# Performance work log

Hardware: AMD Instinct MI355X
Metric: run time of the kernel (lower is better)

The kernel has to match this reference:

```python
import jax, jax.numpy as jnp
import numpy as np

B, S, D, H = 2, 4096, 512, 8
DH = D // H  # head dim = 64


def setup_inputs() -> dict:
    key = jax.random.key(0)
    ks = jax.random.split(key, 5)
    s = 1.0 / np.sqrt(D)
    return {
        "x": jax.random.normal(ks[0], (B, S, D), jnp.float32),
        "Wq": jax.random.normal(ks[1], (D, D), jnp.float32) * s,
        "bq": jnp.zeros((D,), jnp.float32),
        "Wk": jax.random.normal(ks[2], (D, D), jnp.float32) * s,
        "bk": jnp.zeros((D,), jnp.float32),
        "Wv": jax.random.normal(ks[3], (D, D), jnp.float32) * s,
        "bv": jnp.zeros((D,), jnp.float32),
        "Wo": jax.random.normal(ks[4], (D, D), jnp.float32) * s,
        "bo": jnp.zeros((D,), jnp.float32),
    }


def _split_heads(t):  # [B,S,D] -> [B,H,S,DH]
    return t.reshape(B, S, H, DH).transpose(0, 2, 1, 3)


def reference(x, Wq, bq, Wk, bk, Wv, bv, Wo, bo):
    relu = jax.nn.relu
    # linear projections with activation (keras MultiHeadAttention applies
    # the activation to all Q/K/V/output mappings)
    q = _split_heads(relu(x @ Wq + bq))
    k = _split_heads(relu(x @ Wk + bk))
    v = _split_heads(relu(x @ Wv + bv))
    # scaled dot-product attention; scale uses per-head feature dim (DH)
    e = jnp.einsum("bhqd,bhkd->bhqk", q, k) / jnp.sqrt(jnp.float32(DH))
    attn = jax.nn.softmax(e, axis=-1)  # stable max-subtract softmax
    o = jnp.einsum("bhqk,bhkd->bhqd", attn, v)
    o = o.transpose(0, 2, 1, 3).reshape(B, S, D)  # merge heads
    return relu(o @ Wo + bo)
```

## Files before the change

### kernel.cpp

```cpp
#include <hip/hip_runtime.h>
#include <stdint.h>

#define B_ 2
#define S_ 4096
#define D_ 512
#define H_ 8
#define DH_ 64
#define M_ (B_*S_)
#define LOG2E 1.4426950408889634f

typedef unsigned short u16;
typedef __bf16 bf16x8 __attribute__((ext_vector_type(8)));
typedef __bf16 bf16x4 __attribute__((ext_vector_type(4)));
typedef float f32x4 __attribute__((ext_vector_type(4)));

#if defined(__has_builtin)
#if __has_builtin(__builtin_amdgcn_exp2f)
#define EXP2(x) __builtin_amdgcn_exp2f(x)
#else
#define EXP2(x) exp2f(x)
#endif
#else
#define EXP2(x) exp2f(x)
#endif

__device__ __forceinline__ u16 f2bf(float f) {
  __bf16 b = (__bf16)f;
  return __builtin_bit_cast(u16, b);
}

__device__ __forceinline__ void gl_lds16(const void* g, void* l) {
  __builtin_amdgcn_global_load_lds(
      (__attribute__((address_space(1))) void*)(void*)g,
      (__attribute__((address_space(3))) void*)l, 16, 0, 0);
}

#define MM(a, b, c) __builtin_amdgcn_mfma_f32_16x16x32_bf16((a), (b), (c), 0, 0, 0)
#define LD8(p) (*(const bf16x8*)(p))

__global__ void k_prep(const float* __restrict__ x, u16* __restrict__ xb,
                       const float* __restrict__ w0, const float* __restrict__ w1,
                       const float* __restrict__ w2, const float* __restrict__ w3,
                       u16* __restrict__ t0, u16* __restrict__ t1,
                       u16* __restrict__ t2, u16* __restrict__ t3) {
  __shared__ float t[32][33];
  int bid = blockIdx.x, tid = threadIdx.x;
  if (bid < 4096) {
    int i = bid * 256 + tid;
    float4 v = ((const float4*)x)[i];
    bf16x4 o;
    o[0] = (__bf16)v.x; o[1] = (__bf16)v.y; o[2] = (__bf16)v.z; o[3] = (__bf16)v.w;
    ((bf16x4*)xb)[i] = o;
  } else {
    int zb = bid - 4096;
    int z = zb >> 8;
    int rem = zb & 255;
    int bx = rem & 15, by = rem >> 4;
    const float* w = z == 0 ? w0 : z == 1 ? w1 : z == 2 ? w2 : w3;
    u16* wt       = z == 0 ? t0 : z == 1 ? t1 : z == 2 ? t2 : t3;
    int n0 = bx * 32, k0 = by * 32;
    int tx = tid & 31, ty = tid >> 5;
    #pragma unroll
    for (int j = 0; j < 4; j++) t[ty + 8*j][tx] = w[(k0 + ty + 8*j) * D_ + n0 + tx];
    __syncthreads();
    #pragma unroll
    for (int j = 0; j < 4; j++) wt[(n0 + ty + 8*j) * D_ + k0 + tx] = f2bf(t[tx][ty + 8*j]);
  }
}

template<int BUF, int LAST>
__device__ __forceinline__ void gemm_step(
    const u16*& Ap0, const u16*& Ap1, const u16*& Bp0, const u16*& Bp1,
    u16* (&Adst)[2][2], u16* (&Bdst)[2][2],
    const u16* Al0, const u16* Al1, const u16* Bl0, const u16* Bl1,
    const int (&afo)[2][4], const int (&bfo)[2][2], f32x4 (&acc)[4][2]) {
  if (!LAST) {
    gl_lds16(Ap0, Adst[BUF^1][0]);
    gl_lds16(Ap1, Adst[BUF^1][1]);
    gl_lds16(Bp0, Bdst[BUF^1][0]);
    gl_lds16(Bp1, Bdst[BUF^1][1]);
    Ap0 += 64; Ap1 += 64; Bp0 += 64; Bp1 += 64;
    asm volatile("s_waitcnt vmcnt(4)" ::: "memory");
  } else {
    asm volatile("s_waitcnt vmcnt(0)" ::: "memory");
  }
  __builtin_amdgcn_s_barrier();
  __builtin_amdgcn_sched_barrier(0);
  const char* Ab = (const char*)(BUF ? Al1 : Al0);
  const char* Bb = (const char*)(BUF ? Bl1 : Bl0);
  #pragma unroll
  for (int h = 0; h < 2; h++) {
    bf16x8 a0 = LD8(Ab + afo[h][0]);
    bf16x8 a1 = LD8(Ab + afo[h][1]);
    bf16x8 a2 = LD8(Ab + afo[h][2]);
    bf16x8 a3 = LD8(Ab + afo[h][3]);
    bf16x8 b0 = LD8(Bb + bfo[h][0]);
    bf16x8 b1 = LD8(Bb + bfo[h][1]);
    acc[0][0] = MM(a0, b0, acc[0][0]); acc[0][1] = MM(a0, b1, acc[0][1]);
    acc[1][0] = MM(a1, b0, acc[1][0]); acc[1][1] = MM(a1, b1, acc[1][1]);
    acc[2][0] = MM(a2, b0, acc[2][0]); acc[2][1] = MM(a2, b1, acc[2][1]);
    acc[3][0] = MM(a3, b0, acc[3][0]); acc[3][1] = MM(a3, b1, acc[3][1]);
  }
  __builtin_amdgcn_sched_barrier(0);
  __builtin_amdgcn_s_barrier();
}

__device__ __forceinline__
void gemm_body(const u16* __restrict__ A, const u16* __restrict__ Bt,
               const float* __restrict__ bias, void* __restrict__ out,
               float scale, int mode) {
  __shared__ __align__(16) u16 Al[2][128*64];
  __shared__ __align__(16) u16 Bl[2][128*64];
  int tid = threadIdx.x;
  int lane = tid & 63, w = tid >> 6;
  int wr = w >> 2, wc = w & 3;
  int g = lane >> 4, qi = lane & 15, qi7 = qi & 7;
  int m0 = blockIdx.y * 128, n0 = blockIdx.x * 128;
  int swzc = ((lane & 7) ^ (lane >> 3)) * 8;
  int lr8 = lane >> 3;

  f32x4 acc[4][2] = {};

  int afo[2][4], bfo[2][2];
  #pragma unroll
  for (int h = 0; h < 2; h++) {
    #pragma unroll
    for (int i = 0; i < 4; i++)
      afo[h][i] = (wr*64 + i*16 + qi)*128 + (((h*4 + g) ^ qi7)*16);
    #pragma unroll
    for (int jn = 0; jn < 2; jn++)
      bfo[h][jn] = (wc*32 + jn*16 + qi)*128 + (((h*4 + g) ^ qi7)*16);
  }

  const u16* Ap0 = A  + (m0 + w*16 + lr8)*D_ + swzc;
  const u16* Ap1 = Ap0 + 8*D_;
  const u16* Bp0 = Bt + (n0 + w*16 + lr8)*D_ + swzc;
  const u16* Bp1 = Bp0 + 8*D_;
  u16* Adst[2][2];
  u16* Bdst[2][2];
  #pragma unroll
  for (int bb2 = 0; bb2 < 2; bb2++)
    #pragma unroll
    for (int j = 0; j < 2; j++) {
      Adst[bb2][j] = &Al[bb2][(w*16 + j*8)*64];
      Bdst[bb2][j] = &Bl[bb2][(w*16 + j*8)*64];
    }

  gl_lds16(Ap0, Adst[0][0]);
  gl_lds16(Ap1, Adst[0][1]);
  gl_lds16(Bp0, Bdst[0][0]);
  gl_lds16(Bp1, Bdst[0][1]);
  Ap0 += 64; Ap1 += 64; Bp0 += 64; Bp1 += 64;

#define GS(BUF, LAST) gemm_step<BUF, LAST>(Ap0, Ap1, Bp0, Bp1, Adst, Bdst, \
    Al[0], Al[1], Bl[0], Bl[1], afo, bfo, acc)
  GS(0,0); GS(1,0); GS(0,0); GS(1,0); GS(0,0); GS(1,0); GS(0,0); GS(1,1);
#undef GS

  #pragma unroll
  for (int i = 0; i < 4; i++)
    #pragma unroll
    for (int jn = 0; jn < 2; jn++) {
      int col = n0 + wc*32 + jn*16 + qi;
      float bs = bias[col];
      if (mode == 1) {
        int row0 = m0 + wr*64 + i*16 + g*4;
        int bb = row0 >> 12, ss0 = row0 & (S_ - 1);
        int hh = col >> 6, dd = col & 63;
        bf16x4 pk;
        pk[0] = (__bf16)(fmaxf(acc[i][jn][0] + bs, 0.0f) * scale);
        pk[1] = (__bf16)(fmaxf(acc[i][jn][1] + bs, 0.0f) * scale);
        pk[2] = (__bf16)(fmaxf(acc[i][jn][2] + bs, 0.0f) * scale);
        pk[3] = (__bf16)(fmaxf(acc[i][jn][3] + bs, 0.0f) * scale);
        *(bf16x4*)&((u16*)out)[((bb*H_ + hh)*DH_ + dd)*S_ + ss0] = pk;
      } else {
        #pragma unroll
        for (int ii = 0; ii < 4; ii++) {
          int row = m0 + wr*64 + i*16 + g*4 + ii;
          float v = fmaxf(acc[i][jn][ii] + bs, 0.0f) * scale;
          if (mode == 2) {
            ((float*)out)[row * D_ + col] = v;
          } else {
            int bb = row >> 12, ss = row & (S_ - 1);
            int hh = col >> 6, dd = col & 63;
            ((u16*)out)[((bb*H_ + hh)*S_ + ss)*DH_ + dd] = f2bf(v);
          }
        }
      }
    }
}

__global__ __launch_bounds__(512, 2)
void k_qkv(const u16* __restrict__ A,
           const u16* __restrict__ btq, const u16* __restrict__ btk, const u16* __restrict__ btv,
           const float* __restrict__ bq, const float* __restrict__ bk, const float* __restrict__ bv,
           u16* __restrict__ q, u16* __restrict__ k, u16* __restrict__ v) {
  int z = blockIdx.z;
  if (z == 0)      gemm_body(A, btq, bq, q, 0.125f * LOG2E, 0);
  else if (z == 1) gemm_body(A, btk, bk, k, 1.0f, 0);
  else             gemm_body(A, btv, bv, v, 1.0f, 1);
}

__global__ __launch_bounds__(512, 2)
void k_go(const u16* __restrict__ A, const u16* __restrict__ bt,
          const float* __restrict__ bias, float* __restrict__ out) {
  gemm_body(A, bt, bias, out, 1.0f, 2);
}

template<int BUF, int LAST>
__device__ __forceinline__ void attn_tile(
    const u16*& kp0, const u16*& kp1, const u16*& vp0, const u16*& vp1,
    u16* (&kdst)[2][2], u16* (&vdst)[2][2],
    const u16* Kl0, const u16* Kl1, const u16* Vl0, const u16* Vl1,
    char* Pw, const int (&fo)[4][2], const int (&pwo)[4], int pr0, int pr1,
    bf16x8 aqA0, bf16x8 aqA1, bf16x8 aqB0, bf16x8 aqB1,
    f32x4 (&oA)[4], f32x4 (&oB)[4], float& lA, float& lB) {
  if (!LAST) {
    gl_lds16(kp0, kdst[BUF^1][0]);
    gl_lds16(kp1, kdst[BUF^1][1]);
    gl_lds16(vp0, vdst[BUF^1][0]);
    gl_lds16(vp1, vdst[BUF^1][1]);
    kp0 += 64*DH_; kp1 += 64*DH_; vp0 += 64; vp1 += 64;
    asm volatile("s_waitcnt vmcnt(4)" ::: "memory");
  } else {
    asm volatile("s_waitcnt vmcnt(0)" ::: "memory");
  }
  __builtin_amdgcn_s_barrier();
  __builtin_amdgcn_sched_barrier(0);
  const char* Kb = (const char*)(BUF ? Kl1 : Kl0);
  const char* Vb = (const char*)(BUF ? Vl1 : Vl0);
  const f32x4 zro = {0.f, 0.f, 0.f, 0.f};

  f32x4 sA[4], sB[4];
  #pragma unroll
  for (int kt = 0; kt < 4; kt++) {
    bf16x8 k0 = LD8(Kb + fo[kt][0]);
    bf16x8 k1 = LD8(Kb + fo[kt][1]);
    sA[kt] = MM(k1, aqA1, MM(k0, aqA0, zro));
    sB[kt] = MM(k1, aqB1, MM(k0, aqB0, zro));
  }

  float suA = 0.0f, suB = 0.0f;
  #pragma unroll
  for (int kt = 0; kt < 4; kt++) {
    float a0 = EXP2(sA[kt][0]), a1 = EXP2(sA[kt][1]);
    float a2 = EXP2(sA[kt][2]), a3 = EXP2(sA[kt][3]);
    suA += (a0+a1)+(a2+a3);
    bf16x4 pa; pa[0]=(__bf16)a0; pa[1]=(__bf16)a1; pa[2]=(__bf16)a2; pa[3]=(__bf16)a3;
    *(bf16x4*)(Pw + pwo[kt]) = pa;
    float b0 = EXP2(sB[kt][0]), b1 = EXP2(sB[kt][1]);
    float b2 = EXP2(sB[kt][2]), b3 = EXP2(sB[kt][3]);
    suB += (b0+b1)+(b2+b3);
    bf16x4 pb; pb[0]=(__bf16)b0; pb[1]=(__bf16)b1; pb[2]=(__bf16)b2; pb[3]=(__bf16)b3;
    *(bf16x4*)(Pw + 2048 + pwo[kt]) = pb;
  }
  lA += suA; lB += suB;

  __builtin_amdgcn_s_setprio(1);
  #pragma unroll
  for (int kh = 0; kh < 2; kh++) {
    bf16x8 apA = LD8(Pw + (kh ? pr1 : pr0));
    bf16x8 apB = LD8(Pw + 2048 + (kh ? pr1 : pr0));
    #pragma unroll
    for (int nt = 0; nt < 4; nt++) {
      bf16x8 vf = LD8(Vb + fo[nt][kh]);
      oA[nt] = MM(apA, vf, oA[nt]);
      oB[nt] = MM(apB, vf, oB[nt]);
    }
  }
  __builtin_amdgcn_s_setprio(0);
  __builtin_amdgcn_sched_barrier(0);
  __builtin_amdgcn_s_barrier();
}

__global__ __launch_bounds__(256, 2)
void k_attn(const u16* __restrict__ Q, const u16* __restrict__ K,
            const u16* __restrict__ Vt, u16* __restrict__ O) {
  __shared__ __align__(16) u16 Kl[2][64*64];
  __shared__ __align__(16) u16 Vl[2][64*64];
  __shared__ __align__(16) u16 Pl[4][32*64];
  const int tid = threadIdx.x;
  const int lane = tid & 63, w = tid >> 6;
  const int g = lane >> 4, qi = lane & 15, qi7 = qi & 7;

  const int bid = blockIdx.x;
  const int xcd = bid & 7, idx = bid >> 3;
  const int hb = xcd * 2 + (idx & 1);
  const int qt = idx >> 1;
  const int b = hb >> 3, h = hb & 7;

  const u16* Qh = Q  + ((b*H_ + h) * S_) * DH_;
  const u16* Kh = K  + ((b*H_ + h) * S_) * DH_;
  const u16* Vh = Vt + ((b*H_ + h) * DH_) * S_;
  const int q0 = qt*128 + w*32;

  const bf16x8 aqA0 = LD8(&Qh[(q0 + qi)*DH_ + g*8]);
  const bf16x8 aqA1 = LD8(&Qh[(q0 + qi)*DH_ + 32 + g*8]);
  const bf16x8 aqB0 = LD8(&Qh[(q0 + 16 + qi)*DH_ + g*8]);
  const bf16x8 aqB1 = LD8(&Qh[(q0 + 16 + qi)*DH_ + 32 + g*8]);

  f32x4 oA[4] = {}, oB[4] = {};
  float lA = 0.0f, lB = 0.0f;

  const int swzc = ((lane & 7) ^ (lane >> 3)) * 8;
  const int lr8 = lane >> 3;

  int fo[4][2];
  #pragma unroll
  for (int rt = 0; rt < 4; rt++)
    #pragma unroll
    for (int kh = 0; kh < 2; kh++)
      fo[rt][kh] = (rt*16 + qi)*128 + (((kh*4 + g) ^ qi7)*16);
  int pwo[4];
  #pragma unroll
  for (int kt = 0; kt < 4; kt++)
    pwo[kt] = qi*128 + (((kt*2 + (g >> 1)) ^ qi7)*16) + (g & 1)*8;
  const int pr0 = qi*128 + ((g ^ qi7)*16);
  const int pr1 = qi*128 + (((4 + g) ^ qi7)*16);
  char* Pw = (char*)Pl[w];

  const u16* kp0 = Kh + (w*16 + lr8)*DH_ + swzc;
  const u16* kp1 = kp0 + 8*DH_;
  const u16* vp0 = Vh + (w*16 + lr8)*S_ + swzc;
  const u16* vp1 = vp0 + 8*S_;
  u16* kdst[2][2];
  u16* vdst[2][2];
  #pragma unroll
  for (int bb2 = 0; bb2 < 2; bb2++)
    #pragma unroll
    for (int j = 0; j < 2; j++) {
      kdst[bb2][j] = &Kl[bb2][(w*16 + j*8)*64];
      vdst[bb2][j] = &Vl[bb2][(w*16 + j*8)*64];
    }

  gl_lds16(kp0, kdst[0][0]);
  gl_lds16(kp1, kdst[0][1]);
  gl_lds16(vp0, vdst[0][0]);
  gl_lds16(vp1, vdst[0][1]);
  kp0 += 64*DH_; kp1 += 64*DH_; vp0 += 64; vp1 += 64;

#define T(BUF, LAST) attn_tile<BUF, LAST>(kp0, kp1, vp0, vp1, kdst, vdst, \
    &Kl[0][0], &Kl[1][0], &Vl[0][0], &Vl[1][0], Pw, fo, pwo, pr0, pr1, \
    aqA0, aqA1, aqB0, aqB1, oA, oB, lA, lB)

  for (int i = 0; i < 31; ++i) {
    T(0, 0);
    T(1, 0);
  }
  T(0, 0);
  T(1, 1);
#undef T

  lA += __shfl_xor(lA, 16); lA += __shfl_xor(lA, 32);
  lB += __shfl_xor(lB, 16); lB += __shfl_xor(lB, 32);
  float rvA = 1.0f / lA, rvB = 1.0f / lB;
  float rrA[4], rrB[4];
  #pragma unroll
  for (int i = 0; i < 4; i++) {
    rrA[i] = __shfl(rvA, g*4 + i);
    rrB[i] = __shfl(rvB, g*4 + i);
  }
  #pragma unroll
  for (int ii = 0; ii < 4; ii++) {
    int rowA = q0 + g*4 + ii;
    u16* oaro = O + (b*S_ + rowA)*D_ + h*64 + qi;
    oaro[0]  = f2bf(oA[0][ii] * rrA[ii]);
    oaro[16] = f2bf(oA[1][ii] * rrA[ii]);
    oaro[32] = f2bf(oA[2][ii] * rrA[ii]);
    oaro[48] = f2bf(oA[3][ii] * rrA[ii]);
    u16* obro = oaro + 16*D_;
    obro[0]  = f2bf(oB[0][ii] * rrB[ii]);
    obro[16] = f2bf(oB[1][ii] * rrB[ii]);
    obro[32] = f2bf(oB[2][ii] * rrB[ii]);
    obro[48] = f2bf(oB[3][ii] * rrB[ii]);
  }
}

extern "C" void kernel_launch(void* const* d_in, const int* in_sizes, int n_in,
                              void* d_out, int out_size, void* d_ws, size_t ws_size,
                              hipStream_t stream) {
  (void)in_sizes; (void)n_in; (void)out_size; (void)ws_size;
  const float* x  = (const float*)d_in[0];
  const float* Wq = (const float*)d_in[1];
  const float* bq = (const float*)d_in[2];
  const float* Wk = (const float*)d_in[3];
  const float* bk = (const float*)d_in[4];
  const float* Wv = (const float*)d_in[5];
  const float* bv = (const float*)d_in[6];
  const float* Wo = (const float*)d_in[7];
  const float* bo = (const float*)d_in[8];

  char* ws = (char*)d_ws;
  u16* xb  = (u16*)ws;
  u16* wtq = (u16*)(ws + 8388608);
  u16* wtk = wtq + 512*512;
  u16* wtv = wtk + 512*512;
  u16* wto = wtv + 512*512;
  u16* Qh  = (u16*)(ws + 8388608 + 4*524288);
  u16* Kh  = Qh + M_*D_;
  u16* Vt  = Kh + M_*D_;
  u16* Ob  = xb;

  k_prep<<<5120, 256, 0, stream>>>(x, xb, Wq, Wk, Wv, Wo, wtq, wtk, wtv, wto);
  k_qkv<<<dim3(4,64,3), 512, 0, stream>>>(xb, wtq, wtk, wtv, bq, bk, bv, Qh, Kh, Vt);
  k_attn<<<512, 256, 0, stream>>>(Qh, Kh, Vt, Ob);
  k_go<<<dim3(4,64), 512, 0, stream>>>(Ob, wto, bo, (float*)d_out);
}
```

Baseline: 199.4 us.

## Double query rows per attention wave to reuse K/V fragments across four subtiles

Each attention wave now processes 64 query rows (four 16-row subtiles) instead of 32, so a block covers 256 queries and the grid is halved to 256 blocks. Every K and V fragment loaded from LDS feeds twice as many MFMAs, cutting LDS read traffic and K/V streaming per query. The P scratch buffer doubles and launch bounds drop to one block per SIMD. The cost is much higher register pressure and fewer resident waves per CU, which weakens latency hiding. Only one block per CU may be available to overlap the barriers.

```diff
diff --git a/kernel.cpp b/kernel.cpp
--- a/kernel.cpp
+++ b/kernel.cpp
@@ -213,8 +213,7 @@
     u16* (&kdst)[2][2], u16* (&vdst)[2][2],
     const u16* Kl0, const u16* Kl1, const u16* Vl0, const u16* Vl1,
     char* Pw, const int (&fo)[4][2], const int (&pwo)[4], int pr0, int pr1,
-    bf16x8 aqA0, bf16x8 aqA1, bf16x8 aqB0, bf16x8 aqB1,
-    f32x4 (&oA)[4], f32x4 (&oB)[4], float& lA, float& lB) {
+    const bf16x8 (&aq)[4][2], f32x4 (&oo)[4][4], float (&ls)[4]) {
   if (!LAST) {
     gl_lds16(kp0, kdst[BUF^1][0]);
     gl_lds16(kp1, kdst[BUF^1][1]);
@@ -231,41 +230,44 @@
   const char* Vb = (const char*)(BUF ? Vl1 : Vl0);
   const f32x4 zro = {0.f, 0.f, 0.f, 0.f};
 
-  f32x4 sA[4], sB[4];
+  f32x4 s[4][4];
   #pragma unroll
   for (int kt = 0; kt < 4; kt++) {
     bf16x8 k0 = LD8(Kb + fo[kt][0]);
     bf16x8 k1 = LD8(Kb + fo[kt][1]);
-    sA[kt] = MM(k1, aqA1, MM(k0, aqA0, zro));
-    sB[kt] = MM(k1, aqB1, MM(k0, aqB0, zro));
-  }
-
-  float suA = 0.0f, suB = 0.0f;
-  #pragma unroll
-  for (int kt = 0; kt < 4; kt++) {
-    float a0 = EXP2(sA[kt][0]), a1 = EXP2(sA[kt][1]);
-    float a2 = EXP2(sA[kt][2]), a3 = EXP2(sA[kt][3]);
-    suA += (a0+a1)+(a2+a3);
-    bf16x4 pa; pa[0]=(__bf16)a0; pa[1]=(__bf16)a1; pa[2]=(__bf16)a2; pa[3]=(__bf16)a3;
-    *(bf16x4*)(Pw + pwo[kt]) = pa;
-    float b0 = EXP2(sB[kt][0]), b1 = EXP2(sB[kt][1]);
-    float b2 = EXP2(sB[kt][2]), b3 = EXP2(sB[kt][3]);
-    suB += (b0+b1)+(b2+b3);
-    bf16x4 pb; pb[0]=(__bf16)b0; pb[1]=(__bf16)b1; pb[2]=(__bf16)b2; pb[3]=(__bf16)b3;
-    *(bf16x4*)(Pw + 2048 + pwo[kt]) = pb;
-  }
-  lA += suA; lB += suB;
+    #pragma unroll
+    for (int st = 0; st < 4; st++)
+      s[st][kt] = MM(k1, aq[st][1], MM(k0, aq[st][0], zro));
+  }
+
+  #pragma unroll
+  for (int st = 0; st < 4; st++) {
+    float su = 0.0f;
+    #pragma unroll
+    for (int kt = 0; kt < 4; kt++) {
+      float e0 = EXP2(s[st][kt][0]), e1 = EXP2(s[st][kt][1]);
+      float e2 = EXP2(s[st][kt][2]), e3 = EXP2(s[st][kt][3]);
+      su += (e0+e1)+(e2+e3);
+      bf16x4 p; p[0]=(__bf16)e0; p[1]=(__bf16)e1; p[2]=(__bf16)e2; p[3]=(__bf16)e3;
+      *(bf16x4*)(Pw + st*2048 + pwo[kt]) = p;
+    }
+    ls[st] += su;
+  }
 
   __builtin_amdgcn_s_setprio(1);
   #pragma unroll
   for (int kh = 0; kh < 2; kh++) {
-    bf16x8 apA = LD8(Pw + (kh ? pr1 : pr0));
-    bf16x8 apB = LD8(Pw + 2048 + (kh ? pr1 : pr0));
+    bf16x8 ap0 = LD8(Pw +        (kh ? pr1 : pr0));
+    bf16x8 ap1 = LD8(Pw + 2048 + (kh ? pr1 : pr0));
+    bf16x8 ap2 = LD8(Pw + 4096 + (kh ? pr1 : pr0));
+    bf16x8 ap3 = LD8(Pw + 6144 + (kh ? pr1 : pr0));
     #pragma unroll
     for (int nt = 0; nt < 4; nt++) {
       bf16x8 vf = LD8(Vb + fo[nt][kh]);
-      oA[nt] = MM(apA, vf, oA[nt]);
-      oB[nt] = MM(apB, vf, oB[nt]);
+      oo[0][nt] = MM(ap0, vf, oo[0][nt]);
+      oo[1][nt] = MM(ap1, vf, oo[1][nt]);
+      oo[2][nt] = MM(ap2, vf, oo[2][nt]);
+      oo[3][nt] = MM(ap3, vf, oo[3][nt]);
     }
   }
   __builtin_amdgcn_s_setprio(0);
@@ -273,12 +275,12 @@
   __builtin_amdgcn_s_barrier();
 }
 
-__global__ __launch_bounds__(256, 2)
+__global__ __launch_bounds__(256, 1)
 void k_attn(const u16* __restrict__ Q, const u16* __restrict__ K,
             const u16* __restrict__ Vt, u16* __restrict__ O) {
   __shared__ __align__(16) u16 Kl[2][64*64];
   __shared__ __align__(16) u16 Vl[2][64*64];
-  __shared__ __align__(16) u16 Pl[4][32*64];
+  __shared__ __align__(16) u16 Pl[4][64*64];
   const int tid = threadIdx.x;
   const int lane = tid & 63, w = tid >> 6;
   const int g = lane >> 4, qi = lane & 15, qi7 = qi & 7;
@@ -292,15 +294,17 @@
   const u16* Qh = Q  + ((b*H_ + h) * S_) * DH_;
   const u16* Kh = K  + ((b*H_ + h) * S_) * DH_;
   const u16* Vh = Vt + ((b*H_ + h) * DH_) * S_;
-  const int q0 = qt*128 + w*32;
-
-  const bf16x8 aqA0 = LD8(&Qh[(q0 + qi)*DH_ + g*8]);
-  const bf16x8 aqA1 = LD8(&Qh[(q0 + qi)*DH_ + 32 + g*8]);
-  const bf16x8 aqB0 = LD8(&Qh[(q0 + 16 + qi)*DH_ + g*8]);
-  const bf16x8 aqB1 = LD8(&Qh[(q0 + 16 + qi)*DH_ + 32 + g*8]);
-
-  f32x4 oA[4] = {}, oB[4] = {};
-  float lA = 0.0f, lB = 0.0f;
+  const int q0 = qt*256 + w*64;
+
+  bf16x8 aq[4][2];
+  #pragma unroll
+  for (int st = 0; st < 4; st++) {
+    aq[st][0] = LD8(&Qh[(q0 + st*16 + qi)*DH_ + g*8]);
+    aq[st][1] = LD8(&Qh[(q0 + st*16 + qi)*DH_ + 32 + g*8]);
+  }
+
+  f32x4 oo[4][4] = {};
+  float ls[4] = {0.f, 0.f, 0.f, 0.f};
 
   const int swzc = ((lane & 7) ^ (lane >> 3)) * 8;
   const int lr8 = lane >> 3;
@@ -340,8 +344,7 @@
   kp0 += 64*DH_; kp1 += 64*DH_; vp0 += 64; vp1 += 64;
 
 #define T(BUF, LAST) attn_tile<BUF, LAST>(kp0, kp1, vp0, vp1, kdst, vdst, \
-    &Kl[0][0], &Kl[1][0], &Vl[0][0], &Vl[1][0], Pw, fo, pwo, pr0, pr1, \
-    aqA0, aqA1, aqB0, aqB1, oA, oB, lA, lB)
+    &Kl[0][0], &Kl[1][0], &Vl[0][0], &Vl[1][0], Pw, fo, pwo, pr0, pr1, aq, oo, ls)
 
   for (int i = 0; i < 31; ++i) {
     T(0, 0);
@@ -351,28 +354,22 @@
   T(1, 1);
 #undef T
 
-  lA += __shfl_xor(lA, 16); lA += __shfl_xor(lA, 32);
-  lB += __shfl_xor(lB, 16); lB += __shfl_xor(lB, 32);
-  float rvA = 1.0f / lA, rvB = 1.0f / lB;
-  float rrA[4], rrB[4];
-  #pragma unroll
-  for (int i = 0; i < 4; i++) {
-    rrA[i] = __shfl(rvA, g*4 + i);
-    rrB[i] = __shfl(rvB, g*4 + i);
-  }
-  #pragma unroll
-  for (int ii = 0; ii < 4; ii++) {
-    int rowA = q0 + g*4 + ii;
-    u16* oaro = O + (b*S_ + rowA)*D_ + h*64 + qi;
-    oaro[0]  = f2bf(oA[0][ii] * rrA[ii]);
-    oaro[16] = f2bf(oA[1][ii] * rrA[ii]);
-    oaro[32] = f2bf(oA[2][ii] * rrA[ii]);
-    oaro[48] = f2bf(oA[3][ii] * rrA[ii]);
-    u16* obro = oaro + 16*D_;
-    obro[0]  = f2bf(oB[0][ii] * rrB[ii]);
-    obro[16] = f2bf(oB[1][ii] * rrB[ii]);
-    obro[32] = f2bf(oB[2][ii] * rrB[ii]);
-    obro[48] = f2bf(oB[3][ii] * rrB[ii]);
+  #pragma unroll
+  for (int st = 0; st < 4; st++) {
+    float l = ls[st];
+    l += __shfl_xor(l, 16);
+    l += __shfl_xor(l, 32);
+    float rv = 1.0f / l;
+    #pragma unroll
+    for (int ii = 0; ii < 4; ii++) {
+      float rr = __shfl(rv, g*4 + ii);
+      int row = q0 + st*16 + g*4 + ii;
+      u16* orow = O + (b*S_ + row)*D_ + h*64 + qi;
+      orow[0]  = f2bf(oo[st][0][ii] * rr);
+      orow[16] = f2bf(oo[st][1][ii] * rr);
+      orow[32] = f2bf(oo[st][2][ii] * rr);
+      orow[48] = f2bf(oo[st][3][ii] * rr);
+    }
   }
 }
 
@@ -403,6 +400,6 @@
 
   k_prep<<<5120, 256, 0, stream>>>(x, xb, Wq, Wk, Wv, Wo, wtq, wtk, wtv, wto);
   k_qkv<<<dim3(4,64,3), 512, 0, stream>>>(xb, wtq, wtk, wtv, bq, bk, bv, Qh, Kh, Vt);
-  k_attn<<<512, 256, 0, stream>>>(Qh, Kh, Vt, Ob);
+  k_attn<<<256, 256, 0, stream>>>(Qh, Kh, Vt, Ob);
   k_go<<<dim3(4,64), 512, 0, stream>>>(Ob, wto, bo, (float*)d_out);
 }
```

New measurement: 220.5 us. 1.11x slower.
